# Optimization experiments

Measured on AMD Instinct MI355X. Metric: run time of the kernel, lower is better.

The kernel has to match this reference:

```python
import jax, jax.numpy as jnp
import numpy as np

N, M, D, NNZ, H = 1024, 1024, 128, 32768, 256


def setup_inputs() -> dict:
    key = jax.random.key(0)
    k_x, k_v, k_e, k_w1, k_b1, k_w2, k_b2 = jax.random.split(key, 7)
    X = jax.random.normal(k_x, (N, D), dtype=jnp.float32)
    V = jax.random.randint(k_v, (NNZ,), 0, N)
    E = jax.random.randint(k_e, (NNZ,), 0, M)
    # nn.Linear(2D, 256) and nn.Linear(256, 1) params (Kaiming-uniform-ish init)
    lim1 = 1.0 / np.sqrt(2 * D)
    W1 = jax.random.uniform(k_w1, (2 * D, H), minval=-lim1, maxval=lim1, dtype=jnp.float32)
    b1 = jax.random.uniform(k_b1, (H,), minval=-lim1, maxval=lim1, dtype=jnp.float32)
    lim2 = 1.0 / np.sqrt(H)
    W2 = jax.random.uniform(k_w2, (H, 1), minval=-lim2, maxval=lim2, dtype=jnp.float32)
    b2 = jax.random.uniform(k_b2, (1,), minval=-lim2, maxval=lim2, dtype=jnp.float32)
    return {"X": X, "V": V, "E": E, "W1": W1, "b1": b1, "W2": W2, "b2": b2}


def reference(X, V, E, W1, b1, W2, b2):
    # scatter-mean: eX[m] = mean of X[V[j]] over j with E[j] == m  -> [M, D]
    gathered = X[V]  # [NNZ, D]
    sums = jax.ops.segment_sum(gathered, E, num_segments=M)           # [M, D]
    counts = jax.ops.segment_sum(jnp.ones((NNZ,), X.dtype), E, num_segments=M)
    eX = sums / jnp.maximum(counts, 1.0)[:, None]
    # cat([X_broadcast, eX_broadcast], -1) @ W1 == X @ W1[:D] + eX @ W1[D:]
    # avoids materializing the [N, M, 2D] concat; math is identical.
    hx = X @ W1[:D]    # [N, H]
    he = eX @ W1[D:]   # [M, H]
    h = jax.nn.relu(hx[:, None, :] + he[None, :, :] + b1)  # [N, M, H]
    logits = jnp.squeeze(h @ W2, axis=-1) + b2              # [N, M]
    return jax.nn.sigmoid(logits)
```

## Files before the change

kernel.cpp:

```cpp
#include <hip/hip_runtime.h>

#define N_ 1024
#define M_ 1024
#define D_ 128
#define NNZ_ 32768
#define H_ 256
#define BKT_ 96

typedef _Float16 h2 __attribute__((ext_vector_type(2)));

__global__ __launch_bounds__(256) void bucket_kernel(
        const int* __restrict__ V, const int* __restrict__ E,
        int* __restrict__ counts, int* __restrict__ bucket) {
    int j = blockIdx.x * 256 + threadIdx.x;
    int e = E[j];
    int slot = atomicAdd(&counts[e], 1);
    if (slot < BKT_) bucket[e * BKT_ + slot] = V[j];
}

__global__ __launch_bounds__(256) void gemm_kernel(
        const float* __restrict__ X, const int* __restrict__ counts,
        const int* __restrict__ bucket, const float* __restrict__ W1,
        const float* __restrict__ b1,
        _Float16* __restrict__ hx, _Float16* __restrict__ heb) {
    __shared__ float sA[16][128];
    const int t = threadIdx.x;
    const int b = blockIdx.x;

    if (b < 64) {
        const int row0 = b * 16;
        {
            const float4* A4 = (const float4*)(X + row0 * D_);
            float4* S4 = (float4*)&sA[0][0];
            S4[t] = A4[t];
            S4[t + 256] = A4[t + 256];
        }
        __syncthreads();

        float acc[16];
#pragma unroll
        for (int r = 0; r < 16; ++r) acc[r] = 0.f;

        for (int d = 0; d < D_; d += 4) {
            float w0 = W1[(d + 0) * H_ + t];
            float w1 = W1[(d + 1) * H_ + t];
            float w2 = W1[(d + 2) * H_ + t];
            float w3 = W1[(d + 3) * H_ + t];
#pragma unroll
            for (int r = 0; r < 16; ++r) {
                float4 a = *(const float4*)&sA[r][d];
                acc[r] = fmaf(a.x, w0, acc[r]);
                acc[r] = fmaf(a.y, w1, acc[r]);
                acc[r] = fmaf(a.z, w2, acc[r]);
                acc[r] = fmaf(a.w, w3, acc[r]);
            }
        }
#pragma unroll
        for (int r = 0; r < 16; ++r)
            hx[(row0 + r) * H_ + t] = (_Float16)acc[r];
    } else {
        const int m0 = (b - 64) * 8;
        const int d = t & 127;
        const int half = t >> 7;

#pragma unroll
        for (int p = 0; p < 4; ++p) {
            const int r = p * 2 + half;
            const int m = m0 + r;
            const int cnt = min(counts[m], BKT_);
            const int* __restrict__ bk = bucket + m * BKT_;
            float s = 0.f;
            int i = 0;
            for (; i + 4 <= cnt; i += 4) {
                int v0 = bk[i], v1 = bk[i + 1], v2 = bk[i + 2], v3 = bk[i + 3];
                s += X[v0 * D_ + d];
                s += X[v1 * D_ + d];
                s += X[v2 * D_ + d];
                s += X[v3 * D_ + d];
            }
            for (; i < cnt; ++i) s += X[bk[i] * D_ + d];
            sA[r][d] = s;
        }
        __syncthreads();

        float acc[8];
#pragma unroll
        for (int r = 0; r < 8; ++r) acc[r] = 0.f;

        const float* __restrict__ W = W1 + D_ * H_;
        for (int dd = 0; dd < D_; dd += 4) {
            float w0 = W[(dd + 0) * H_ + t];
            float w1 = W[(dd + 1) * H_ + t];
            float w2 = W[(dd + 2) * H_ + t];
            float w3 = W[(dd + 3) * H_ + t];
#pragma unroll
            for (int r = 0; r < 8; ++r) {
                float4 a = *(const float4*)&sA[r][dd];
                acc[r] = fmaf(a.x, w0, acc[r]);
                acc[r] = fmaf(a.y, w1, acc[r]);
                acc[r] = fmaf(a.z, w2, acc[r]);
                acc[r] = fmaf(a.w, w3, acc[r]);
            }
        }

        const float bias = b1[t];
#pragma unroll
        for (int r = 0; r < 8; ++r) {
            float inv = 1.0f / fmaxf((float)counts[m0 + r], 1.0f);
            heb[(m0 + r) * H_ + t] = (_Float16)(acc[r] * inv + bias);
        }
    }
}

__global__ __launch_bounds__(512) void big_kernel(
        const _Float16* __restrict__ hx, const _Float16* __restrict__ heb,
        const float* __restrict__ W2, const float* __restrict__ b2,
        float* __restrict__ out) {
    __shared__ _Float16 sA[64][264];
    __shared__ _Float16 sB[64][264];
    __shared__ h2 sW[H_ / 2];

    const int tid = threadIdx.x;
    const int tx = tid & 15;
    const int ty = tid >> 4;
    const int n0 = blockIdx.y * 64;
    const int m0 = blockIdx.x * 64;

    if (tid < H_ / 2) {
        h2 w;
        w.x = (_Float16)W2[2 * tid];
        w.y = (_Float16)W2[2 * tid + 1];
        sW[tid] = w;
    }

    {
        const float4* A4 = (const float4*)hx;
        const float4* B4 = (const float4*)heb;
#pragma unroll
        for (int it = 0; it < 4; ++it) {
            int lin = it * 512 + tid;
            int row = lin >> 5;
            int c = lin & 31;
            *(float4*)&sA[row][c * 8] = A4[(n0 + row) * 32 + c];
            *(float4*)&sB[row][c * 8] = B4[(m0 + row) * 32 + c];
        }
    }
    __syncthreads();

    float acc[2][4];
#pragma unroll
    for (int i = 0; i < 2; ++i)
#pragma unroll
        for (int j = 0; j < 4; ++j) acc[i][j] = 0.f;

    union V { float4 f4; h2 h[4]; };
    const h2 z = {(_Float16)0.f, (_Float16)0.f};

#pragma unroll 4
    for (int hp = 0; hp < H_ / 2; hp += 4) {
        V av[2], bv[4], wv;
        wv.f4 = *(const float4*)&sW[hp];
#pragma unroll
        for (int i = 0; i < 2; ++i) av[i].f4 = *(const float4*)&sA[ty + 32 * i][hp * 2];
#pragma unroll
        for (int j = 0; j < 4; ++j) bv[j].f4 = *(const float4*)&sB[tx + 16 * j][hp * 2];
#pragma unroll
        for (int k = 0; k < 4; ++k) {
#pragma unroll
            for (int i = 0; i < 2; ++i) {
#pragma unroll
                for (int j = 0; j < 4; ++j) {
                    h2 t = av[i].h[k] + bv[j].h[k];
                    t = __builtin_elementwise_max(t, z);
                    acc[i][j] = __builtin_amdgcn_fdot2(t, wv.h[k], acc[i][j], false);
                }
            }
        }
    }

    const float bb = b2[0];
#pragma unroll
    for (int i = 0; i < 2; ++i) {
#pragma unroll
        for (int j = 0; j < 4; ++j) {
            float x = acc[i][j] + bb;
            out[(n0 + ty + 32 * i) * M_ + (m0 + tx + 16 * j)] =
                1.0f / (1.0f + __expf(-x));
        }
    }
}

extern "C" void kernel_launch(void* const* d_in, const int* in_sizes, int n_in,
                              void* d_out, int out_size, void* d_ws, size_t ws_size,
                              hipStream_t stream) {
    const float* X  = (const float*)d_in[0];
    const int*   V  = (const int*)d_in[1];
    const int*   E  = (const int*)d_in[2];
    const float* W1 = (const float*)d_in[3];
    const float* b1 = (const float*)d_in[4];
    const float* W2 = (const float*)d_in[5];
    const float* b2 = (const float*)d_in[6];
    float* out = (float*)d_out;

    char* ws = (char*)d_ws;
    int*      counts = (int*)(ws);
    int*      bucket = (int*)(ws + 4096);
    _Float16* hx     = (_Float16*)(ws + 397312);
    _Float16* heb    = (_Float16*)(ws + 921600);

    hipMemsetAsync(counts, 0, M_ * sizeof(int), stream);

    bucket_kernel<<<NNZ_ / 256, 256, 0, stream>>>(V, E, counts, bucket);

    gemm_kernel<<<192, 256, 0, stream>>>(X, counts, bucket, W1, b1, hx, heb);

    dim3 bgrid(M_ / 64, N_ / 64);
    big_kernel<<<bgrid, 512, 0, stream>>>(hx, heb, W2, b2, out);
}
```

Measured before the change: 113.1 us.

## Fuse scatter bucketing into gemm kernel using per-block LDS buckets

Drops the memset and the separate global-atomic bucket kernel. Each eX block now scans the whole E/V arrays itself and builds its 8 segment buckets in shared memory with LDS atomics. This removes two launches and the global atomic traffic. In exchange, each of the 128 eX blocks reads all 256KB of E and V redundantly, and per-segment capacity is capped at 128 (raised from 96).

```diff
diff --git a/kernel.cpp b/kernel.cpp
--- a/kernel.cpp
+++ b/kernel.cpp
@@ -5,25 +5,17 @@
 #define D_ 128
 #define NNZ_ 32768
 #define H_ 256
-#define BKT_ 96
 
 typedef _Float16 h2 __attribute__((ext_vector_type(2)));
 
-__global__ __launch_bounds__(256) void bucket_kernel(
-        const int* __restrict__ V, const int* __restrict__ E,
-        int* __restrict__ counts, int* __restrict__ bucket) {
-    int j = blockIdx.x * 256 + threadIdx.x;
-    int e = E[j];
-    int slot = atomicAdd(&counts[e], 1);
-    if (slot < BKT_) bucket[e * BKT_ + slot] = V[j];
-}
-
 __global__ __launch_bounds__(256) void gemm_kernel(
-        const float* __restrict__ X, const int* __restrict__ counts,
-        const int* __restrict__ bucket, const float* __restrict__ W1,
+        const float* __restrict__ X, const int* __restrict__ V,
+        const int* __restrict__ E, const float* __restrict__ W1,
         const float* __restrict__ b1,
         _Float16* __restrict__ hx, _Float16* __restrict__ heb) {
     __shared__ float sA[16][128];
+    __shared__ int s_bkt[8][128];
+    __shared__ int s_cnt[8];
     const int t = threadIdx.x;
     const int b = blockIdx.x;
 
@@ -60,25 +52,48 @@
             hx[(row0 + r) * H_ + t] = (_Float16)acc[r];
     } else {
         const int m0 = (b - 64) * 8;
+
+        if (t < 8) s_cnt[t] = 0;
+        __syncthreads();
+
+        {
+            const int4* E4 = (const int4*)E;
+            const int4* V4 = (const int4*)V;
+#pragma unroll 4
+            for (int it = 0; it < NNZ_ / 4 / 256; ++it) {
+                int idx = it * 256 + t;
+                int4 e4 = E4[idx];
+                int4 v4 = V4[idx];
+                unsigned r;
+                r = (unsigned)(e4.x - m0);
+                if (r < 8u) { int s = atomicAdd(&s_cnt[r], 1); s_bkt[r][s & 127] = v4.x; }
+                r = (unsigned)(e4.y - m0);
+                if (r < 8u) { int s = atomicAdd(&s_cnt[r], 1); s_bkt[r][s & 127] = v4.y; }
+                r = (unsigned)(e4.z - m0);
+                if (r < 8u) { int s = atomicAdd(&s_cnt[r], 1); s_bkt[r][s & 127] = v4.z; }
+                r = (unsigned)(e4.w - m0);
+                if (r < 8u) { int s = atomicAdd(&s_cnt[r], 1); s_bkt[r][s & 127] = v4.w; }
+            }
+        }
+        __syncthreads();
+
         const int d = t & 127;
         const int half = t >> 7;
-
 #pragma unroll
         for (int p = 0; p < 4; ++p) {
             const int r = p * 2 + half;
-            const int m = m0 + r;
-            const int cnt = min(counts[m], BKT_);
-            const int* __restrict__ bk = bucket + m * BKT_;
+            const int cnt = min(s_cnt[r], 128);
             float s = 0.f;
             int i = 0;
             for (; i + 4 <= cnt; i += 4) {
-                int v0 = bk[i], v1 = bk[i + 1], v2 = bk[i + 2], v3 = bk[i + 3];
+                int v0 = s_bkt[r][i], v1 = s_bkt[r][i + 1];
+                int v2 = s_bkt[r][i + 2], v3 = s_bkt[r][i + 3];
                 s += X[v0 * D_ + d];
                 s += X[v1 * D_ + d];
                 s += X[v2 * D_ + d];
                 s += X[v3 * D_ + d];
             }
-            for (; i < cnt; ++i) s += X[bk[i] * D_ + d];
+            for (; i < cnt; ++i) s += X[s_bkt[r][i] * D_ + d];
             sA[r][d] = s;
         }
         __syncthreads();
@@ -106,7 +121,7 @@
         const float bias = b1[t];
 #pragma unroll
         for (int r = 0; r < 8; ++r) {
-            float inv = 1.0f / fmaxf((float)counts[m0 + r], 1.0f);
+            float inv = 1.0f / fmaxf((float)s_cnt[r], 1.0f);
             heb[(m0 + r) * H_ + t] = (_Float16)(acc[r] * inv + bias);
         }
     }
@@ -153,12 +168,12 @@
 #pragma unroll
         for (int j = 0; j < 4; ++j) acc[i][j] = 0.f;
 
-    union V { float4 f4; h2 h[4]; };
+    union Vn { float4 f4; h2 h[4]; };
     const h2 z = {(_Float16)0.f, (_Float16)0.f};
 
 #pragma unroll 4
     for (int hp = 0; hp < H_ / 2; hp += 4) {
-        V av[2], bv[4], wv;
+        Vn av[2], bv[4], wv;
         wv.f4 = *(const float4*)&sW[hp];
 #pragma unroll
         for (int i = 0; i < 2; ++i) av[i].f4 = *(const float4*)&sA[ty + 32 * i][hp * 2];
@@ -203,16 +218,10 @@
     float* out = (float*)d_out;
 
     char* ws = (char*)d_ws;
-    int*      counts = (int*)(ws);
-    int*      bucket = (int*)(ws + 4096);
-    _Float16* hx     = (_Float16*)(ws + 397312);
-    _Float16* heb    = (_Float16*)(ws + 921600);
-
-    hipMemsetAsync(counts, 0, M_ * sizeof(int), stream);
-
-    bucket_kernel<<<NNZ_ / 256, 256, 0, stream>>>(V, E, counts, bucket);
-
-    gemm_kernel<<<192, 256, 0, stream>>>(X, counts, bucket, W1, b1, hx, heb);
+    _Float16* hx  = (_Float16*)(ws);
+    _Float16* heb = (_Float16*)(ws + 524288);
+
+    gemm_kernel<<<192, 256, 0, stream>>>(X, V, E, W1, b1, hx, heb);
 
     dim3 bgrid(M_ / 64, N_ / 64);
     big_kernel<<<bgrid, 512, 0, stream>>>(hx, heb, W2, b2, out);
```

Measured after the change: 112.2 us. No clear change (-0.8%).
